# Kernel optimization log

Hardware: AMD Instinct MI355X
Metric: run time of the kernel (lower is better)

Reference implementation:

```python
import jax, jax.numpy as jnp
import numpy as np

D_MODEL = 1024
NUM_HEADS = 16
D_HEAD = D_MODEL // NUM_HEADS
MAX_SEQ_LEN = 2048
THETA = 10000.0
BATCH = 2
SEQ = 2048


def _rope_tables():
    # inv_freq over even dims; emb interleaves each freq twice: [f0,f0,f1,f1,...]
    inv_freq = 1.0 / (THETA ** (jnp.arange(0, D_HEAD, 2, dtype=jnp.float32) / D_HEAD))
    t = jnp.arange(MAX_SEQ_LEN, dtype=jnp.float32)
    freqs = jnp.einsum('i,j->ij', t, inv_freq)  # [S, d_head/2]
    emb = jnp.stack((freqs, freqs), axis=-1).reshape(MAX_SEQ_LEN, D_HEAD)
    return jnp.cos(emb), jnp.sin(emb)


def _rotate_half(x):
    # pairwise interleaved rotation: (x0,x1,x2,x3,...) -> (-x1,x0,-x3,x2,...)
    xr = x.reshape(x.shape[:-1] + (D_HEAD // 2, 2))
    x1, x2 = xr[..., 0], xr[..., 1]
    return jnp.stack((-x2, x1), axis=-1).reshape(x.shape)


def setup_inputs() -> dict:
    key = jax.random.key(0)
    ks = jax.random.split(key, 5)
    std = np.sqrt(2.0 / (D_MODEL + D_MODEL)).astype(np.float32)
    return {
        'in_features': jax.random.normal(ks[0], (BATCH, SEQ, D_MODEL), dtype=jnp.float32),
        'token_positions': jnp.arange(SEQ, dtype=jnp.int64) if jax.config.jax_enable_x64 else jnp.arange(SEQ, dtype=jnp.int32),
        'wq': jax.random.normal(ks[1], (D_MODEL, D_MODEL), dtype=jnp.float32) * std,
        'wk': jax.random.normal(ks[2], (D_MODEL, D_MODEL), dtype=jnp.float32) * std,
        'wv': jax.random.normal(ks[3], (D_MODEL, D_MODEL), dtype=jnp.float32) * std,
        'wo': jax.random.normal(ks[4], (D_MODEL, D_MODEL), dtype=jnp.float32) * std,
    }


def reference(in_features, token_positions, wq, wk, wv, wo):
    b, s, _ = in_features.shape
    cos_tab, sin_tab = _rope_tables()
    cos = cos_tab[token_positions]  # [s, d_head]
    sin = sin_tab[token_positions]

    def split_heads(t):  # [b, s, d_model] -> [b, h, s, d_head]
        return t.reshape(b, s, NUM_HEADS, D_HEAD).transpose(0, 2, 1, 3)

    q = split_heads(jnp.einsum('bsd,ed->bse', in_features, wq))
    k = split_heads(jnp.einsum('bsd,ed->bse', in_features, wk))
    v = split_heads(jnp.einsum('bsd,ed->bse', in_features, wv))

    q = q * cos + _rotate_half(q) * sin
    k = k * cos + _rotate_half(k) * sin

    scale = 1.0 / np.sqrt(D_HEAD).astype(np.float32)
    scores = jnp.einsum('bhqd,bhkd->bhqk', q, k) * scale  # [b,h,s,s]
    causal = jnp.tril(jnp.ones((s, s), dtype=bool))
    scores = jnp.where(causal, scores, -jnp.inf)
    weights = jax.nn.softmax(scores, axis=-1)
    out = jnp.einsum('bhqk,bhkd->bhqd', weights, v)
    out = out.transpose(0, 2, 1, 3).reshape(b, s, D_MODEL)
    return jnp.einsum('bsd,ed->bse', out, wo)
```

## Files before the change

kernel.cpp:

```cpp
#include <hip/hip_runtime.h>


typedef __attribute__((ext_vector_type(8))) short bf16x8;
typedef __attribute__((ext_vector_type(4))) float f32x4;

__device__ __forceinline__ short f2bf(float f) {
  unsigned u = __float_as_uint(f);
  unsigned r = (u + 0x7fffu + ((u >> 16) & 1u)) >> 16;
  return (short)(r & 0xFFFFu);
}

__device__ __forceinline__ unsigned pk2rne(float a, float b) {
  return ((unsigned)(unsigned short)f2bf(b) << 16) | (unsigned short)f2bf(a);
}

__device__ __forceinline__ unsigned pk2(float a, float b) {
  return __builtin_amdgcn_perm(__float_as_uint(b) + 0x8000u,
                               __float_as_uint(a) + 0x8000u, 0x07060302u);
}

__device__ __forceinline__ float exp2x(float x) {
  float r;
  asm("v_exp_f32 %0, %1" : "=v"(r) : "v"(x));
  return r;
}

__device__ __forceinline__ void async16(const void* g, void* l) {
  __builtin_amdgcn_global_load_lds(
      (const __attribute__((address_space(1))) void*)g,
      (__attribute__((address_space(3))) void*)l, 16, 0, 0);
}

__device__ __forceinline__ void cstore(short* C, size_t i, float v) { C[i] = f2bf(v); }
__device__ __forceinline__ void cstore(float* C, size_t i, float v) { C[i] = v; }

__global__ void cast_all(const float4* __restrict__ X,
                         const float4* __restrict__ w0, const float4* __restrict__ w1,
                         const float4* __restrict__ w2, const float4* __restrict__ w3,
                         short* __restrict__ Xb, short* __restrict__ Wb) {
  int t = blockIdx.x * 256 + threadIdx.x;
  const float4* s;
  short4* d;
  if (t < (1 << 20)) {
    s = X + t; d = (short4*)Xb + t;
  } else {
    int u = t - (1 << 20);
    int which = u >> 18;
    s = ((which == 0) ? w0 : (which == 1) ? w1 : (which == 2) ? w2 : w3) + (u & 0x3FFFF);
    d = (short4*)Wb + u;
  }
  float4 v = *s;
  *d = make_short4(f2bf(v.x), f2bf(v.y), f2bf(v.z), f2bf(v.w));
}

enum EpiMode { EPI_ROW, EPI_KFRAG, EPI_VFRAG };

template <typename OUT, int MR, int NR, bool ROPE, EpiMode EM, bool MAPB>
__device__ __forceinline__ void gemm_core(short* __restrict__ As, short* __restrict__ Bs,
                                          const short* __restrict__ A, const short* __restrict__ B,
                                          OUT* __restrict__ C, int bm, int bn, int ldc,
                                          const int* __restrict__ pos) {
  constexpr int BM = 32 * MR, BN = 32 * NR;
  constexpr int NLD = (BM * 4 + BN * 4) / 256;
  const int tid  = threadIdx.x;
  const int lane = tid & 63, wave = tid >> 6;
  const int col  = lane & 15, quad = lane >> 4;
  const int wm = (wave & 1) * (16 * MR), wn = (wave >> 1) * (16 * NR);

  f32x4 acc[MR][NR];
#pragma unroll
  for (int i = 0; i < MR; i++)
#pragma unroll
    for (int j = 0; j < NR; j++) acc[i][j] = (f32x4){0.f, 0.f, 0.f, 0.f};

  auto stage = [&](int k0, int bu) {
#pragma unroll
    for (int c = tid; c < BM * 4; c += 256) {
      int r = c >> 2, cc = (c & 3) << 3;
      async16(A + (size_t)(bm + r) * 1024 + k0 + cc, As + bu * BM * 32 + c * 8);
    }
#pragma unroll
    for (int c = tid; c < BN * 4; c += 256) {
      int r = c >> 2, cc = (c & 3) << 3;
      int rg = bn + r;
      if (MAPB) {
        int k6 = rg & 63;
        rg = (rg & ~63) | ((k6 < 32) ? (k6 << 1) : (((k6 - 32) << 1) | 1));
      }
      async16(B + (size_t)rg * 1024 + k0 + cc, Bs + bu * BN * 32 + c * 8);
    }
  };

  stage(0, 0);
  stage(32, 1);
  if constexpr (NLD == 4) asm volatile("s_waitcnt vmcnt(4)" ::: "memory");
  else                    asm volatile("s_waitcnt vmcnt(3)" ::: "memory");
  __builtin_amdgcn_s_barrier();

  int cur = 0, nxt = 2;
  for (int it = 0; it < 32; ++it) {
    if (it < 30) stage((it + 2) * 32, nxt);
    const short* as = As + cur * (BM * 32);
    const short* bs = Bs + cur * (BN * 32);

    bf16x8 af[MR], bfr[NR];
#pragma unroll
    for (int i = 0; i < MR; i++)
      af[i] = *(const bf16x8*)(as + (wm + i * 16 + col) * 32 + quad * 8);
#pragma unroll
    for (int i = 0; i < NR; i++)
      bfr[i] = *(const bf16x8*)(bs + (wn + i * 16 + col) * 32 + quad * 8);
#pragma unroll
    for (int mi = 0; mi < MR; mi++)
#pragma unroll
      for (int ni = 0; ni < NR; ni++)
        acc[mi][ni] = __builtin_amdgcn_mfma_f32_16x16x32_bf16(af[mi], bfr[ni], acc[mi][ni], 0, 0, 0);

    if (it < 30) {
      if constexpr (NLD == 4) asm volatile("s_waitcnt vmcnt(4)" ::: "memory");
      else                    asm volatile("s_waitcnt vmcnt(3)" ::: "memory");
    } else {
      asm volatile("s_waitcnt vmcnt(0)" ::: "memory");
    }
    __builtin_amdgcn_s_barrier();
    cur = (cur == 2) ? 0 : cur + 1;
    nxt = (nxt == 2) ? 0 : nxt + 1;
  }

  if (ROPE) {
    float invf[2];
#pragma unroll
    for (int ni = 0; ni < 2; ni++) {
      int p = ni * 16 + col;
      invf[ni] = exp2f(-0.4152410118609203f * (float)p) * 0.15915494309189535f;
    }
#pragma unroll
    for (int mi = 0; mi < MR; mi++) {
#pragma unroll
      for (int r = 0; r < 4; r++) {
        int row = bm + wm + mi * 16 + quad * 4 + r;
        float fp = (float)pos[row & 2047];
#pragma unroll
        for (int ni = 0; ni < 2; ni++) {
          float rev = fp * invf[ni];
          rev -= floorf(rev);
          float sn = __builtin_amdgcn_sinf(rev);
          float cs = __builtin_amdgcn_cosf(rev);
          float x  = acc[mi][ni][r];
          float yv = acc[mi][ni + 2][r];
          acc[mi][ni][r]     = fmaf(x, cs, -yv * sn);
          acc[mi][ni + 2][r] = fmaf(yv, cs, x * sn);
        }
      }
    }
  }

  if (EM == EPI_ROW) {
#pragma unroll
    for (int mi = 0; mi < MR; mi++) {
#pragma unroll
      for (int r = 0; r < 4; r++) {
        size_t row = (size_t)(bm + wm + mi * 16 + quad * 4 + r);
#pragma unroll
        for (int ni = 0; ni < NR; ni++) {
          int cg = bn + wn + ni * 16 + col;
          cstore(C, row * ldc + cg, acc[mi][ni][r]);
        }
      }
    }
  }
}

__global__ __launch_bounds__(256, 1) void qkv_gemm(const short* __restrict__ Xb,
                                                   const short* __restrict__ Wq,
                                                   const short* __restrict__ Wk,
                                                   const short* __restrict__ Wv,
                                                   short* __restrict__ Qo,
                                                   short* __restrict__ Kf,
                                                   short* __restrict__ Vf,
                                                   const int* __restrict__ pos) {
  __shared__ __align__(16) short sm[49152];
  short* As  = sm;
  short* Bqs = sm + 12288;
  short* Bks = sm + 24576;
  short* Bvs = sm + 36864;

  const int bm = blockIdx.x * 128, bn = blockIdx.y * 128;
  const int tid  = threadIdx.x;
  const int lane = tid & 63, wave = tid >> 6;
  const int col  = lane & 15, quad = lane >> 4;
  const int wm = (wave & 1) * 64, wn = (wave >> 1) * 64;

  f32x4 aq[4][4], ak[4][4], av[4][4];
#pragma unroll
  for (int i = 0; i < 4; i++)
#pragma unroll
    for (int j = 0; j < 4; j++) {
      aq[i][j] = (f32x4){0.f, 0.f, 0.f, 0.f};
      ak[i][j] = (f32x4){0.f, 0.f, 0.f, 0.f};
      av[i][j] = (f32x4){0.f, 0.f, 0.f, 0.f};
    }

  auto stage = [&](int k0, int bu) {
#pragma unroll
    for (int c = tid; c < 512; c += 256) {
      int r = c >> 2, cc = (c & 3) << 3;
      async16(Xb + (size_t)(bm + r) * 1024 + k0 + cc, As + bu * 4096 + c * 8);
    }
#pragma unroll
    for (int c = tid; c < 512; c += 256) {
      int r = c >> 2, cc = (c & 3) << 3;
      int rg = bn + r;
      int k6 = rg & 63;
      int rp = (rg & ~63) | ((k6 < 32) ? (k6 << 1) : (((k6 - 32) << 1) | 1));
      async16(Wq + (size_t)rp * 1024 + k0 + cc, Bqs + bu * 4096 + c * 8);
      async16(Wk + (size_t)rp * 1024 + k0 + cc, Bks + bu * 4096 + c * 8);
      async16(Wv + (size_t)rg * 1024 + k0 + cc, Bvs + bu * 4096 + c * 8);
    }
  };

  stage(0, 0);
  stage(32, 1);
  asm volatile("s_waitcnt vmcnt(8)" ::: "memory");
  __builtin_amdgcn_s_barrier();

  int cur = 0, nxt = 2;
  for (int it = 0; it < 32; ++it) {
    if (it < 30) stage((it + 2) * 32, nxt);
    const short* as = As + cur * 4096;
    const short* bq = Bqs + cur * 4096;
    const short* bk = Bks + cur * 4096;
    const short* bv = Bvs + cur * 4096;

    bf16x8 af[4], bfq[4], bfk[4], bfv[4];
#pragma unroll
    for (int i = 0; i < 4; i++)
      af[i] = *(const bf16x8*)(as + (wm + i * 16 + col) * 32 + quad * 8);
#pragma unroll
    for (int i = 0; i < 4; i++) {
      bfq[i] = *(const bf16x8*)(bq + (wn + i * 16 + col) * 32 + quad * 8);
      bfk[i] = *(const bf16x8*)(bk + (wn + i * 16 + col) * 32 + quad * 8);
      bfv[i] = *(const bf16x8*)(bv + (wn + i * 16 + col) * 32 + quad * 8);
    }
#pragma unroll
    for (int mi = 0; mi < 4; mi++)
#pragma unroll
      for (int ni = 0; ni < 4; ni++) {
        aq[mi][ni] = __builtin_amdgcn_mfma_f32_16x16x32_bf16(af[mi], bfq[ni], aq[mi][ni], 0, 0, 0);
        ak[mi][ni] = __builtin_amdgcn_mfma_f32_16x16x32_bf16(af[mi], bfk[ni], ak[mi][ni], 0, 0, 0);
        av[mi][ni] = __builtin_amdgcn_mfma_f32_16x16x32_bf16(af[mi], bfv[ni], av[mi][ni], 0, 0, 0);
      }

    if (it < 30) asm volatile("s_waitcnt vmcnt(8)" ::: "memory");
    else         asm volatile("s_waitcnt vmcnt(0)" ::: "memory");
    __builtin_amdgcn_s_barrier();
    cur = (cur == 2) ? 0 : cur + 1;
    nxt = (nxt == 2) ? 0 : nxt + 1;
  }

  float invf[2];
#pragma unroll
  for (int ni = 0; ni < 2; ni++) {
    int p = ni * 16 + col;
    invf[ni] = exp2f(-0.4152410118609203f * (float)p) * 0.15915494309189535f;
  }
#pragma unroll
  for (int mi = 0; mi < 4; mi++) {
#pragma unroll
    for (int r = 0; r < 4; r++) {
      int row = bm + wm + mi * 16 + quad * 4 + r;
      float fp = (float)pos[row & 2047];
#pragma unroll
      for (int ni = 0; ni < 2; ni++) {
        float rev = fp * invf[ni];
        rev -= floorf(rev);
        float sn = __builtin_amdgcn_sinf(rev);
        float cs = __builtin_amdgcn_cosf(rev);
        float xq = aq[mi][ni][r], yq = aq[mi][ni + 2][r];
        aq[mi][ni][r]     = fmaf(xq, cs, -yq * sn);
        aq[mi][ni + 2][r] = fmaf(yq, cs, xq * sn);
        float xk = ak[mi][ni][r], yk = ak[mi][ni + 2][r];
        ak[mi][ni][r]     = fmaf(xk, cs, -yk * sn);
        ak[mi][ni + 2][r] = fmaf(yk, cs, xk * sn);
      }
    }
  }

#pragma unroll
  for (int mi = 0; mi < 4; mi++) {
#pragma unroll
    for (int r = 0; r < 4; r++) {
      size_t row = (size_t)(bm + wm + mi * 16 + quad * 4 + r);
#pragma unroll
      for (int ni = 0; ni < 4; ni++) {
        int cg = bn + wn + ni * 16 + col;
        Qo[row * 1024 + cg] = f2bf(aq[mi][ni][r]);
      }
    }
  }
#pragma unroll
  for (int mi = 0; mi < 4; mi++) {
#pragma unroll
    for (int r = 0; r < 4; r++) {
      int m = bm + wm + mi * 16 + quad * 4 + r;
      int bq2 = m >> 11, key = m & 2047;
      int kt = key >> 6, nb = (key >> 4) & 3, cl = key & 15;
#pragma unroll
      for (int ni = 0; ni < 4; ni++) {
        int e = bn + wn + ni * 16 + col;
        int h = e >> 6, d = e & 63;
        size_t seg = ((((size_t)(bq2 * 16 + h) * 32 + kt) * 4 + nb) * 2 + (d >> 5));
        Kf[seg * 512 + (((d >> 3) & 3) * 16 + cl) * 8 + (d & 7)] = f2bf(ak[mi][ni][r]);
      }
    }
  }
  {
    const int k7base = (quad & 1) * 4;
#pragma unroll
    for (int mi = 0; mi < 4; mi++) {
      int m0 = bm + wm + mi * 16 + quad * 4;
      int bq2 = m0 >> 11, key = m0 & 2047;
      int kt = key >> 6;
      int k16 = (mi * 2 + (quad >> 1)) & 3;
      int half = mi >> 1;
#pragma unroll
      for (int ni = 0; ni < 4; ni++) {
        int e = bn + wn + ni * 16 + col;
        int h = e >> 6, d = e & 63;
        int nb = d >> 4, cl = d & 15;
        size_t seg = ((((size_t)(bq2 * 16 + h) * 32 + kt) * 4 + nb) * 2 + half);
        size_t off = seg * 512 + (size_t)(k16 * 16 + cl) * 8 + k7base;
        *(uint2*)(Vf + off) = make_uint2(pk2rne(av[mi][ni][0], av[mi][ni][1]),
                                         pk2rne(av[mi][ni][2], av[mi][ni][3]));
      }
    }
  }
}

__global__ __launch_bounds__(256) void out_gemm(const short* __restrict__ Ctx,
                                                const short* __restrict__ Wo,
                                                float* __restrict__ C) {
  __shared__ __align__(16) short sm[3 * 128 * 32 + 3 * 128 * 32];
  gemm_core<float, 4, 4, false, EPI_ROW, false>(sm, sm + 3 * 128 * 32, Ctx, Wo, C,
                                                blockIdx.x * 128, blockIdx.y * 128, 1024, nullptr);
}

__global__ __launch_bounds__(256, 3) void flash_attn(const short* __restrict__ Q,
                                                     const short* __restrict__ Kf,
                                                     const short* __restrict__ Vf,
                                                     short* __restrict__ ctx) {
  const int y = blockIdx.y;
  const int g = y >> 3, r8 = y & 7;
  const int qt = (g == 0) ? 31 - r8 : (g == 1) ? r8 : (g == 2) ? 23 - r8 : 8 + r8;
  const int bh = blockIdx.x;
  const int b = bh >> 4, h = bh & 15;
  __shared__ __align__(16) short Ps[4][16 * 72];
  __shared__ __align__(16) short Ksm[2][4096];
  __shared__ __align__(16) short Vsm[2][4096];
  const int tid = threadIdx.x, lane = tid & 63, wave = tid >> 6;
  const int col = lane & 15, quad = lane >> 4;

  const short* Kg = Kf + (size_t)bh * 131072;
  const short* Vg = Vf + (size_t)bh * 131072;

  const float C1 = 0.18033688011112042f;
  const float mC2 = -17.31234049066756f;

  short* myPs = &Ps[wave][0];
  const int cx = col & 3;
  const int pswr0 = col * 72 + ((0 ^ cx) << 4) + quad * 4;
  const int pswr1 = col * 72 + ((1 ^ cx) << 4) + quad * 4;
  const int pswr2 = col * 72 + ((2 ^ cx) << 4) + quad * 4;
  const int pswr3 = col * 72 + ((3 ^ cx) << 4) + quad * 4;
  const int psrd0 = col * 72 + (((quad >> 1) ^ cx) << 4) + (quad & 1) * 8;
  const int psrd1 = col * 72 + ((((quad >> 1) + 2) ^ cx) << 4) + (quad & 1) * 8;

  auto stageKV = [&](int kt, short* kb, short* vb) {
    const short* kg = Kg + kt * 4096;
    const short* vg = Vg + kt * 4096;
#pragma unroll
    for (int c = tid; c < 512; c += 256) {
      async16(kg + c * 8, kb + c * 8);
      async16(vg + c * 8, vb + c * 8);
    }
  };

  const size_t qrow = (size_t)(b * 2048 + qt * 64 + wave * 16 + col);
  bf16x8 qf0 = *(const bf16x8*)(Q + qrow * 1024 + h * 64 + quad * 8);
  bf16x8 qf1 = *(const bf16x8*)(Q + qrow * 1024 + h * 64 + 32 + quad * 8);

  float l_i = 0.f;
  f32x4 o_acc[4];
#pragma unroll
  for (int i = 0; i < 4; i++) o_acc[i] = (f32x4){0.f, 0.f, 0.f, 0.f};

  short *kcur = &Ksm[0][0], *vcur = &Vsm[0][0];
  short *knxt = &Ksm[1][0], *vnxt = &Vsm[1][0];

  stageKV(0, kcur, vcur);
  asm volatile("s_waitcnt vmcnt(0)" ::: "memory");
  __builtin_amdgcn_s_barrier();

  bf16x8 afp0 = (bf16x8){0,0,0,0,0,0,0,0}, afp1 = (bf16x8){0,0,0,0,0,0,0,0};
  bf16x8 vfp[4][2];
#pragma unroll
  for (int i = 0; i < 4; i++) vfp[i][0] = vfp[i][1] = (bf16x8){0,0,0,0,0,0,0,0};

  for (int kt = 0; kt < qt; ++kt) {
    stageKV(kt + 1, knxt, vnxt);

    bf16x8 kfr[4][2];
#pragma unroll
    for (int nb = 0; nb < 4; nb++) {
      kfr[nb][0] = *(const bf16x8*)(kcur + (nb * 2 + 0) * 512 + lane * 8);
      kfr[nb][1] = *(const bf16x8*)(kcur + (nb * 2 + 1) * 512 + lane * 8);
    }

    f32x4 s_acc[4];
    __builtin_amdgcn_s_setprio(1);
#pragma unroll
    for (int nb = 0; nb < 4; nb++) {
      f32x4 z = (f32x4){0.f, 0.f, 0.f, 0.f};
      z = __builtin_amdgcn_mfma_f32_16x16x32_bf16(kfr[nb][0], qf0, z, 0, 0, 0);
      z = __builtin_amdgcn_mfma_f32_16x16x32_bf16(kfr[nb][1], qf1, z, 0, 0, 0);
      s_acc[nb] = z;
    }
    if (kt > 0) {
#pragma unroll
      for (int nb = 0; nb < 4; nb++) {
        o_acc[nb] = __builtin_amdgcn_mfma_f32_16x16x32_bf16(afp0, vfp[nb][0], o_acc[nb], 0, 0, 0);
        o_acc[nb] = __builtin_amdgcn_mfma_f32_16x16x32_bf16(afp1, vfp[nb][1], o_acc[nb], 0, 0, 0);
      }
    }
    __builtin_amdgcn_s_setprio(0);

#pragma unroll
    for (int nb = 0; nb < 4; nb++) {
      vfp[nb][0] = *(const bf16x8*)(vcur + (nb * 2 + 0) * 512 + lane * 8);
      vfp[nb][1] = *(const bf16x8*)(vcur + (nb * 2 + 1) * 512 + lane * 8);
    }

#pragma unroll
    for (int nb = 0; nb < 4; nb++) {
      float p0 = exp2x(fmaf(s_acc[nb][0], C1, mC2));
      float p1 = exp2x(fmaf(s_acc[nb][1], C1, mC2));
      float p2 = exp2x(fmaf(s_acc[nb][2], C1, mC2));
      float p3 = exp2x(fmaf(s_acc[nb][3], C1, mC2));
      int wr = (nb == 0) ? pswr0 : (nb == 1) ? pswr1 : (nb == 2) ? pswr2 : pswr3;
      *(uint2*)(myPs + wr) = make_uint2(pk2(p0, p1), pk2(p2, p3));
      l_i += (p0 + p1) + (p2 + p3);
    }
    afp0 = *(const bf16x8*)(myPs + psrd0);
    afp1 = *(const bf16x8*)(myPs + psrd1);

    asm volatile("s_waitcnt vmcnt(0)" ::: "memory");
    __builtin_amdgcn_s_barrier();
    short* t;
    t = kcur; kcur = knxt; knxt = t;
    t = vcur; vcur = vnxt; vnxt = t;
  }

  {
    const int ql = wave * 16 + col;
    const int kl = quad * 4;

    bf16x8 kfr[4][2];
#pragma unroll
    for (int nb = 0; nb < 4; nb++) {
      kfr[nb][0] = *(const bf16x8*)(kcur + (nb * 2 + 0) * 512 + lane * 8);
      kfr[nb][1] = *(const bf16x8*)(kcur + (nb * 2 + 1) * 512 + lane * 8);
    }

    f32x4 s_acc[4];
    __builtin_amdgcn_s_setprio(1);
#pragma unroll
    for (int nb = 0; nb < 4; nb++) {
      f32x4 z = (f32x4){0.f, 0.f, 0.f, 0.f};
      z = __builtin_amdgcn_mfma_f32_16x16x32_bf16(kfr[nb][0], qf0, z, 0, 0, 0);
      z = __builtin_amdgcn_mfma_f32_16x16x32_bf16(kfr[nb][1], qf1, z, 0, 0, 0);
      s_acc[nb] = z;
    }
    if (qt > 0) {
#pragma unroll
      for (int nb = 0; nb < 4; nb++) {
        o_acc[nb] = __builtin_amdgcn_mfma_f32_16x16x32_bf16(afp0, vfp[nb][0], o_acc[nb], 0, 0, 0);
        o_acc[nb] = __builtin_amdgcn_mfma_f32_16x16x32_bf16(afp1, vfp[nb][1], o_acc[nb], 0, 0, 0);
      }
    }
    __builtin_amdgcn_s_setprio(0);

#pragma unroll
    for (int nb = 0; nb < 4; nb++) {
      vfp[nb][0] = *(const bf16x8*)(vcur + (nb * 2 + 0) * 512 + lane * 8);
      vfp[nb][1] = *(const bf16x8*)(vcur + (nb * 2 + 1) * 512 + lane * 8);
    }

#pragma unroll
    for (int nb = 0; nb < 4; nb++) {
      float pv[4];
#pragma unroll
      for (int r = 0; r < 4; r++) {
        pv[r] = exp2x(fmaf(s_acc[nb][r], C1, mC2));
        if ((nb * 16 + kl + r) > ql) pv[r] = 0.f;
      }
      int wr = (nb == 0) ? pswr0 : (nb == 1) ? pswr1 : (nb == 2) ? pswr2 : pswr3;
      *(uint2*)(myPs + wr) = make_uint2(pk2(pv[0], pv[1]), pk2(pv[2], pv[3]));
      l_i += (pv[0] + pv[1]) + (pv[2] + pv[3]);
    }
    afp0 = *(const bf16x8*)(myPs + psrd0);
    afp1 = *(const bf16x8*)(myPs + psrd1);

    __builtin_amdgcn_s_setprio(1);
#pragma unroll
    for (int nb = 0; nb < 4; nb++) {
      o_acc[nb] = __builtin_amdgcn_mfma_f32_16x16x32_bf16(afp0, vfp[nb][0], o_acc[nb], 0, 0, 0);
      o_acc[nb] = __builtin_amdgcn_mfma_f32_16x16x32_bf16(afp1, vfp[nb][1], o_acc[nb], 0, 0, 0);
    }
    __builtin_amdgcn_s_setprio(0);
  }

  l_i += __shfl_xor(l_i, 16);
  l_i += __shfl_xor(l_i, 32);
  float invl = 1.0f / l_i;

#pragma unroll
  for (int r = 0; r < 4; r++) {
    float inv = __shfl(invl, quad * 4 + r);
    size_t row = (size_t)(b * 2048 + qt * 64 + wave * 16 + quad * 4 + r);
#pragma unroll
    for (int nb = 0; nb < 4; nb++)
      ctx[row * 1024 + h * 64 + nb * 16 + col] = f2bf(o_acc[nb][r] * inv);
  }
}

extern "C" void kernel_launch(void* const* d_in, const int* in_sizes, int n_in,
                              void* d_out, int out_size, void* d_ws, size_t ws_size,
                              hipStream_t stream) {
  const float* X  = (const float*)d_in[0];
  const int* pos  = (const int*)d_in[1];
  const float* wq = (const float*)d_in[2];
  const float* wk = (const float*)d_in[3];
  const float* wv = (const float*)d_in[4];
  const float* wo = (const float*)d_in[5];
  float* out = (float*)d_out;

  short* Xb  = (short*)d_ws;
  short* Wqb = Xb + (1 << 22);
  short* Wkb = Wqb + (1 << 20);
  short* Wvb = Wkb + (1 << 20);
  short* Wob = Wvb + (1 << 20);
  short* Qb  = Wob + (1 << 20);
  short* Kfb = Qb + (1 << 22);
  short* Vfb = Kfb + (1 << 22);
  short* Ctx = Vfb + (1 << 22);

  cast_all<<<8192, 256, 0, stream>>>((const float4*)X, (const float4*)wq, (const float4*)wk,
                                     (const float4*)wv, (const float4*)wo, Xb, Wqb);
  qkv_gemm<<<dim3(32, 8), 256, 0, stream>>>(Xb, Wqb, Wkb, Wvb, Qb, Kfb, Vfb, pos);
  flash_attn<<<dim3(32, 32), 256, 0, stream>>>(Qb, Kfb, Vfb, Ctx);
  out_gemm<<<dim3(32, 8), 256, 0, stream>>>(Ctx, Wob, out);
}
```

Baseline: 168.8 us.

## Double-buffer QKV GEMM for two blocks per CU, halve out_gemm tile

The QKV projection kernel moves from a triple-buffered LDS pipeline (96 KB) to double buffering (64 KB), with launch bounds raised to two blocks per CU and MFMA sections wrapped in s_setprio. The output projection uses 64-row tiles, doubling its grid from 256 to 512 blocks so more CUs stay busy. The unused RoPE branch is also removed from gemm_core. The trade-off is a shallower prefetch pipeline with a full vmcnt(0) wait every iteration, plus more register pressure in a kernel holding three 4x4 accumulator sets.

```diff
diff --git a/kernel.cpp b/kernel.cpp
--- a/kernel.cpp
+++ b/kernel.cpp
@@ -127,34 +127,6 @@
     nxt = (nxt == 2) ? 0 : nxt + 1;
   }
 
-  if (ROPE) {
-    float invf[2];
-#pragma unroll
-    for (int ni = 0; ni < 2; ni++) {
-      int p = ni * 16 + col;
-      invf[ni] = exp2f(-0.4152410118609203f * (float)p) * 0.15915494309189535f;
-    }
-#pragma unroll
-    for (int mi = 0; mi < MR; mi++) {
-#pragma unroll
-      for (int r = 0; r < 4; r++) {
-        int row = bm + wm + mi * 16 + quad * 4 + r;
-        float fp = (float)pos[row & 2047];
-#pragma unroll
-        for (int ni = 0; ni < 2; ni++) {
-          float rev = fp * invf[ni];
-          rev -= floorf(rev);
-          float sn = __builtin_amdgcn_sinf(rev);
-          float cs = __builtin_amdgcn_cosf(rev);
-          float x  = acc[mi][ni][r];
-          float yv = acc[mi][ni + 2][r];
-          acc[mi][ni][r]     = fmaf(x, cs, -yv * sn);
-          acc[mi][ni + 2][r] = fmaf(yv, cs, x * sn);
-        }
-      }
-    }
-  }
-
   if (EM == EPI_ROW) {
 #pragma unroll
     for (int mi = 0; mi < MR; mi++) {
@@ -171,7 +143,7 @@
   }
 }
 
-__global__ __launch_bounds__(256, 1) void qkv_gemm(const short* __restrict__ Xb,
+__global__ __launch_bounds__(256, 2) void qkv_gemm(const short* __restrict__ Xb,
                                                    const short* __restrict__ Wq,
                                                    const short* __restrict__ Wk,
                                                    const short* __restrict__ Wv,
@@ -179,11 +151,11 @@
                                                    short* __restrict__ Kf,
                                                    short* __restrict__ Vf,
                                                    const int* __restrict__ pos) {
-  __shared__ __align__(16) short sm[49152];
+  __shared__ __align__(16) short sm[32768];
   short* As  = sm;
-  short* Bqs = sm + 12288;
-  short* Bks = sm + 24576;
-  short* Bvs = sm + 36864;
+  short* Bqs = sm + 8192;
+  short* Bks = sm + 16384;
+  short* Bvs = sm + 24576;
 
   const int bm = blockIdx.x * 128, bn = blockIdx.y * 128;
   const int tid  = threadIdx.x;
@@ -220,13 +192,13 @@
   };
 
   stage(0, 0);
-  stage(32, 1);
-  asm volatile("s_waitcnt vmcnt(8)" ::: "memory");
+  asm volatile("s_waitcnt vmcnt(0)" ::: "memory");
   __builtin_amdgcn_s_barrier();
 
-  int cur = 0, nxt = 2;
   for (int it = 0; it < 32; ++it) {
-    if (it < 30) stage((it + 2) * 32, nxt);
+    const int cur = it & 1;
+    if (it < 31) stage((it + 1) * 32, cur ^ 1);
+
     const short* as = As + cur * 4096;
     const short* bq = Bqs + cur * 4096;
     const short* bk = Bks + cur * 4096;
@@ -242,6 +214,7 @@
       bfk[i] = *(const bf16x8*)(bk + (wn + i * 16 + col) * 32 + quad * 8);
       bfv[i] = *(const bf16x8*)(bv + (wn + i * 16 + col) * 32 + quad * 8);
     }
+    __builtin_amdgcn_s_setprio(1);
 #pragma unroll
     for (int mi = 0; mi < 4; mi++)
 #pragma unroll
@@ -250,12 +223,12 @@
         ak[mi][ni] = __builtin_amdgcn_mfma_f32_16x16x32_bf16(af[mi], bfk[ni], ak[mi][ni], 0, 0, 0);
         av[mi][ni] = __builtin_amdgcn_mfma_f32_16x16x32_bf16(af[mi], bfv[ni], av[mi][ni], 0, 0, 0);
       }
-
-    if (it < 30) asm volatile("s_waitcnt vmcnt(8)" ::: "memory");
-    else         asm volatile("s_waitcnt vmcnt(0)" ::: "memory");
-    __builtin_amdgcn_s_barrier();
-    cur = (cur == 2) ? 0 : cur + 1;
-    nxt = (nxt == 2) ? 0 : nxt + 1;
+    __builtin_amdgcn_s_setprio(0);
+
+    if (it < 31) {
+      asm volatile("s_waitcnt vmcnt(0)" ::: "memory");
+      __builtin_amdgcn_s_barrier();
+    }
   }
 
   float invf[2];
@@ -340,9 +313,9 @@
 __global__ __launch_bounds__(256) void out_gemm(const short* __restrict__ Ctx,
                                                 const short* __restrict__ Wo,
                                                 float* __restrict__ C) {
-  __shared__ __align__(16) short sm[3 * 128 * 32 + 3 * 128 * 32];
-  gemm_core<float, 4, 4, false, EPI_ROW, false>(sm, sm + 3 * 128 * 32, Ctx, Wo, C,
-                                                blockIdx.x * 128, blockIdx.y * 128, 1024, nullptr);
+  __shared__ __align__(16) short sm[3 * 64 * 32 + 3 * 128 * 32];
+  gemm_core<float, 2, 4, false, EPI_ROW, false>(sm, sm + 3 * 64 * 32, Ctx, Wo, C,
+                                                blockIdx.x * 64, blockIdx.y * 128, 1024, nullptr);
 }
 
 __global__ __launch_bounds__(256, 3) void flash_attn(const short* __restrict__ Q,
@@ -558,5 +531,5 @@
                                      (const float4*)wv, (const float4*)wo, Xb, Wqb);
   qkv_gemm<<<dim3(32, 8), 256, 0, stream>>>(Xb, Wqb, Wkb, Wvb, Qb, Kfb, Vfb, pos);
   flash_attn<<<dim3(32, 32), 256, 0, stream>>>(Qb, Kfb, Vfb, Ctx);
-  out_gemm<<<dim3(32, 8), 256, 0, stream>>>(Ctx, Wob, out);
-}
+  out_gemm<<<dim3(64, 8), 256, 0, stream>>>(Ctx, Wob, out);
+}
```

Measured after the change: 223.4 us. 1.32x slower.
